# Kernel optimization log

Hardware: AMD Instinct MI355X
Metric: run time of the kernel (lower is better)

## Reference

```python
import jax, jax.numpy as jnp
import numpy as np

B = 8388608  # batch of ODE states
Z_DIM = 4    # [q0, q1, qd0, qd1]


def _potential_sum(q, k1, k2):
    # V = 0.5*k1*q0^2 + 0.5*k2*(q0 - q1)^2, summed over the batch (matches _potential_E)
    return jnp.sum(0.5 * k1[0] * q[:, 0] ** 2 + 0.5 * k2[0] * (q[:, 0] - q[:, 1]) ** 2)


def setup_inputs() -> dict:
    key = jax.random.key(0)
    kx, = jax.random.split(key, 1)
    return {
        "t": jnp.zeros((1,), dtype=jnp.float32),
        "x": jax.random.normal(kx, (B, Z_DIM), dtype=jnp.float32),
        "k1": jnp.ones((1,), dtype=jnp.float32),
        "k2": jnp.ones((1,), dtype=jnp.float32),
    }


def reference(t, x, k1, k2):
    n = x.shape[1] // 2
    q = x[:, :n]    # positions  [B, n]
    qd = x[:, n:]   # velocities [B, n]

    # T = 0.5 * sum(qd^2)  =>  DL_qd = dT/dqd = qd
    # Hessian of DL_qd wrt (q, qd) is [0_{n x n} | I_{n x n}],
    # so DDL_qqd = 0 and DDL_qdqd = I; inv(I) = I.
    # DL_q = d(-V)/dq
    DL_q = -jax.grad(_potential_sum, argnums=0)(q, k1, k2)  # [B, n]

    eye = jnp.eye(n, dtype=x.dtype)  # DDL_qdqd^{-1} (same for every batch element)
    # qdd = einsum('ijk, ij -> ik', DDL_qdqd_inverse, DL_q) with DDL_qdqd_inverse = I
    qdd = jnp.einsum('jk,ij->ik', eye, DL_q)  # [B, n]

    return jnp.concatenate([qd, qdd], axis=1)  # [B, 2n]
```

## Files before the change

### kernel.cpp

```cpp
#include <hip/hip_runtime.h>


typedef float f32x4 __attribute__((ext_vector_type(4)));

#define ROWS_PER_THREAD 4
#define BLOCK 256

__global__ __launch_bounds__(BLOCK) void lagrangian_ode_kernel(
    const f32x4* __restrict__ x,
    const float* __restrict__ k1p,
    const float* __restrict__ k2p,
    f32x4* __restrict__ out,
    int n_rows) {
    const float k1 = k1p[0];
    const float k2 = k2p[0];
    const int base = blockIdx.x * (BLOCK * ROWS_PER_THREAD) + threadIdx.x;

    f32x4 v[ROWS_PER_THREAD];
    int idx[ROWS_PER_THREAD];

#pragma unroll
    for (int r = 0; r < ROWS_PER_THREAD; ++r) {
        idx[r] = base + r * BLOCK;
        if (idx[r] < n_rows) {
            v[r] = x[idx[r]];
        }
    }

#pragma unroll
    for (int r = 0; r < ROWS_PER_THREAD; ++r) {
        if (idx[r] < n_rows) {
            const float d = v[r].x - v[r].y;
            f32x4 o;
            o.x = v[r].z;
            o.y = v[r].w;
            o.z = -(k1 * v[r].x + k2 * d);
            o.w = k2 * d;
            out[idx[r]] = o;
        }
    }
}

extern "C" void kernel_launch(void* const* d_in, const int* in_sizes, int n_in,
                              void* d_out, int out_size, void* d_ws, size_t ws_size,
                              hipStream_t stream) {
    const f32x4* x  = (const f32x4*)d_in[1];
    const float* k1 = (const float*)d_in[2];
    const float* k2 = (const float*)d_in[3];
    f32x4* out = (f32x4*)d_out;

    int n_rows = in_sizes[1] / 4;
    int rows_per_block = BLOCK * ROWS_PER_THREAD;
    int grid = (n_rows + rows_per_block - 1) / rows_per_block;
    lagrangian_ode_kernel<<<grid, BLOCK, 0, stream>>>(x, k1, k2, out, n_rows);
}
```

Before: 237.5 us.

## Software-pipeline row loads with nontemporal stores and larger per-thread work

```diff
diff --git a/kernel.cpp b/kernel.cpp
--- a/kernel.cpp
+++ b/kernel.cpp
@@ -3,8 +3,19 @@
 
 typedef float f32x4 __attribute__((ext_vector_type(4)));
 
-#define ROWS_PER_THREAD 4
 #define BLOCK 256
+#define RPT   16
+#define BATCH 4
+
+__device__ __forceinline__ f32x4 ode(const f32x4 t, const float k1, const float k2) {
+    const float d = t.x - t.y;
+    f32x4 o;
+    o.x = t.z;
+    o.y = t.w;
+    o.z = -(k1 * t.x + k2 * d);
+    o.w = k2 * d;
+    return o;
+}
 
 __global__ __launch_bounds__(BLOCK) void lagrangian_ode_kernel(
     const f32x4* __restrict__ x,
@@ -14,29 +25,37 @@
     int n_rows) {
     const float k1 = k1p[0];
     const float k2 = k2p[0];
-    const int base = blockIdx.x * (BLOCK * ROWS_PER_THREAD) + threadIdx.x;
+    const int chunk = BLOCK * RPT;
+    const int base  = blockIdx.x * chunk + threadIdx.x;
 
-    f32x4 v[ROWS_PER_THREAD];
-    int idx[ROWS_PER_THREAD];
+    if (base + (RPT - 1) * BLOCK < n_rows) {
+        f32x4 v[BATCH], w[BATCH];
+#pragma unroll
+        for (int r = 0; r < BATCH; ++r) v[r] = x[base + r * BLOCK];
 
 #pragma unroll
-    for (int r = 0; r < ROWS_PER_THREAD; ++r) {
-        idx[r] = base + r * BLOCK;
-        if (idx[r] < n_rows) {
-            v[r] = x[idx[r]];
+        for (int k = 1; k < RPT / BATCH; ++k) {
+#pragma unroll
+            for (int r = 0; r < BATCH; ++r)
+                w[r] = x[base + (k * BATCH + r) * BLOCK];
+#pragma unroll
+            for (int r = 0; r < BATCH; ++r)
+                __builtin_nontemporal_store(ode(v[r], k1, k2),
+                                            &out[base + ((k - 1) * BATCH + r) * BLOCK]);
+#pragma unroll
+            for (int r = 0; r < BATCH; ++r) v[r] = w[r];
         }
-    }
-
 #pragma unroll
-    for (int r = 0; r < ROWS_PER_THREAD; ++r) {
-        if (idx[r] < n_rows) {
-            const float d = v[r].x - v[r].y;
-            f32x4 o;
-            o.x = v[r].z;
-            o.y = v[r].w;
-            o.z = -(k1 * v[r].x + k2 * d);
-            o.w = k2 * d;
-            out[idx[r]] = o;
+        for (int r = 0; r < BATCH; ++r)
+            __builtin_nontemporal_store(ode(v[r], k1, k2),
+                                        &out[base + (RPT - BATCH + r) * BLOCK]);
+    } else {
+#pragma unroll
+        for (int j = 0; j < RPT; ++j) {
+            const int i = base + j * BLOCK;
+            if (i < n_rows) {
+                __builtin_nontemporal_store(ode(x[i], k1, k2), &out[i]);
+            }
         }
     }
 }
@@ -50,7 +69,7 @@
     f32x4* out = (f32x4*)d_out;
 
     int n_rows = in_sizes[1] / 4;
-    int rows_per_block = BLOCK * ROWS_PER_THREAD;
+    int rows_per_block = BLOCK * RPT;
     int grid = (n_rows + rows_per_block - 1) / rows_per_block;
     lagrangian_ode_kernel<<<grid, BLOCK, 0, stream>>>(x, k1, k2, out, n_rows);
 }
```

Result: no change. 242.3 us (+2.0%).
